# Kernel tuning notes

Measured on AMD Instinct MI355X. Metric: run time of the kernel, lower is better.

Reference implementation:

```python
import jax, jax.numpy as jnp
import numpy as np

COMMITMENT_LOSS_WEIGHT = 0.25


def setup_inputs() -> dict:
    key = jax.random.key(0)
    k1, k2 = jax.random.split(key)
    B, H, W, C = 64, 32, 32, 256
    D, K = H * W, 1024  # embedding_dim = H*W per the rearrange+reshape in call()
    x = jax.random.normal(k1, (B, H, W, C), dtype=jnp.float32)
    # Orthogonal initializer (like tf.keras.initializers.Orthogonal) via QR
    E = jnp.linalg.qr(jax.random.normal(k2, (D, K), dtype=jnp.float32))[0]
    return {"x": x, "embeddings": E.astype(jnp.float32)}


def reference(x, embeddings):
    B, H, W, C = x.shape
    D = H * W  # embedding_dim
    # einops: 'b h w c -> b c (h w)'
    cont = jnp.transpose(x, (0, 3, 1, 2)).reshape(B, C, D)
    flat = cont.reshape(-1, D)  # [B*C, D]
    # squared L2 distances via norm + matmul (as in get_discretised)
    dists = (jnp.sum(flat * flat, axis=1, keepdims=True)
             + jnp.sum(embeddings * embeddings, axis=0)
             - 2.0 * (flat @ embeddings))  # [B*C, K]
    idx = jnp.argmin(dists, axis=1)  # [B*C]
    # one_hot @ embeddings.T == direct gather of codebook columns
    quantised = embeddings.T[idx].reshape(B, C, D)
    codebook_loss = jnp.mean((jax.lax.stop_gradient(cont) - quantised) ** 2)
    commitment_loss = COMMITMENT_LOSS_WEIGHT * jnp.mean(
        (cont - jax.lax.stop_gradient(quantised)) ** 2)
    loss = codebook_loss + commitment_loss  # layer add_loss terms, summed
    # einops: 'b c (h w) -> b h w c'
    q_bhwc = jnp.transpose(quantised.reshape(B, C, H, W), (0, 2, 3, 1))
    discretised = idx.reshape(-1, C)  # [B, C]
    # straight-through estimator
    q_out = x + jax.lax.stop_gradient(q_bhwc - x)
    return q_out, discretised, loss
```

## Files before the change

### kernel.cpp

```cpp
#include <hip/hip_runtime.h>
#include <float.h>
#include <stdint.h>

#define B_   64
#define C_   256
#define D_   1024
#define K_   1024
#define M_   16384
#define NX_  16777216
#define DISC_OFF NX_
#define LOSS_OFF (NX_ + M_)

typedef _Float16 h8 __attribute__((ext_vector_type(8)));
typedef float    f4 __attribute__((ext_vector_type(4)));

#define XSCALE 512.0f
#define ESCALE 2048.0f
#define DOT_UNSCALE_2 (2.0f / 1048576.0f)

#define WS_EH  0
#define WS_EL  524288
#define WS_CN  1048576
#define WS_PCN 1049600
#define WS_PV  1180672
#define WS_PI  1246208

__device__ __forceinline__ void async16(const _Float16* g, _Float16* l) {
    __builtin_amdgcn_global_load_lds(
        (const __attribute__((address_space(1))) unsigned int*)g,
        (__attribute__((address_space(3))) unsigned int*)l, 16, 0, 0);
}

__global__ __launch_bounds__(256) void split_kernel(const float* __restrict__ x,
                                                    const float* __restrict__ E,
                                                    _Float16* __restrict__ Xh,
                                                    _Float16* __restrict__ Xl,
                                                    _Float16* __restrict__ Eh,
                                                    _Float16* __restrict__ El,
                                                    float* __restrict__ pcn) {
    const int bid = blockIdx.x;
    if (bid < 512) {
        const int tid = bid * 256 + threadIdx.x;
        const int n   = tid & 1023;
        const int o   = tid >> 10;
        const int d0  = o * 8;
        h8 hh, ll;
        float s = 0.f;
        #pragma unroll
        for (int i = 0; i < 8; ++i) {
            const float v = E[(size_t)(d0 + i) * K_ + n];
            s = fmaf(v, v, s);
            const float vs = v * ESCALE;
            const _Float16 h = (_Float16)vs;
            hh[i] = h;
            ll[i] = (_Float16)(vs - (float)h);
        }
        pcn[o * K_ + n] = s;
        const int nt   = n >> 4;
        const int kt   = o >> 2;
        const int lane = (n & 15) + (o & 3) * 16;
        const size_t off = ((size_t)(nt * 32 + kt) * 64 + lane) * 8;
        *(h8*)(Eh + off) = hh;
        *(h8*)(El + off) = ll;
    } else {
        const int tid = (bid - 512) * 256 + threadIdx.x;
        const int m   = tid & 16383;
        const int o   = tid >> 14;
        const int b   = m >> 8, c = m & 255;
        const int d0  = o * 8;
        const float* xp = x + ((size_t)(b * 1024 + d0) * 256) + c;
        h8 hh, ll;
        #pragma unroll
        for (int i = 0; i < 8; ++i) {
            const float v  = xp[(size_t)i * 256];
            const float vs = v * XSCALE;
            const _Float16 h = (_Float16)vs;
            hh[i] = h;
            ll[i] = (_Float16)(vs - (float)h);
        }
        const int mt   = m >> 4;
        const int kt   = o >> 2;
        const int lane = (m & 15) + (o & 3) * 16;
        const size_t off = ((size_t)(mt * 32 + kt) * 64 + lane) * 8;
        *(h8*)(Xh + off) = hh;
        *(h8*)(Xl + off) = ll;
    }
}

__global__ __launch_bounds__(256) void colnorm2_kernel(const float* __restrict__ pcn,
                                                       float* __restrict__ cn,
                                                       float* __restrict__ loss_slot) {
    const int k = blockIdx.x * 256 + threadIdx.x;
    float s = 0.f;
    for (int i = 0; i < 128; ++i) s += pcn[i * K_ + k];
    cn[k] = s;
    if (k == 0) *loss_slot = 0.0f;
}

__global__ __launch_bounds__(512, 2) void gemm_argmin_kernel(
        const _Float16* __restrict__ Xh, const _Float16* __restrict__ Xl,
        const _Float16* __restrict__ Eh, const _Float16* __restrict__ El,
        const float* __restrict__ cn,
        float* __restrict__ pV, int* __restrict__ pI) {
    extern __shared__ _Float16 smem[];
    _Float16* Ab0 = smem;
    _Float16* Ab1 = smem + 8192;
    _Float16* Bb0 = smem + 16384;
    _Float16* Bb1 = smem + 32768;
    float* cV = (float*)(smem + 49152);
    int*   cI = (int*)(cV + 512);

    const int t    = threadIdx.x;
    const int rt   = blockIdx.x >> 2;
    const int ct   = blockIdx.x & 3;
    const int wave = t >> 6, lane = t & 63;
    const int lo16 = lane & 15, hi4 = lane >> 4;
    const int mq   = (wave & 1) * 64;
    const int nq   = (wave >> 1) * 64;
    const int mt0  = rt * 8, nt0 = ct * 16;
    const int n0g  = ct * 256;

    const _Float16* src[6];
    _Float16* dst0[6];
    _Float16* dst1[6];
    #pragma unroll
    for (int i = 0; i < 6; ++i) {
        const int id = wave * 6 + i;
        if (id < 16) {
            const int plane = id >> 3, mt = id & 7;
            src[i]  = (plane ? Xl : Xh) + ((size_t)(mt0 + mt) * 32) * 512 + lane * 8;
            dst0[i] = Ab0 + (plane * 8 + mt) * 512 + lane * 8;
            dst1[i] = Ab1 + (plane * 8 + mt) * 512 + lane * 8;
        } else {
            const int q = id - 16;
            const int plane = q >> 4, nt = q & 15;
            src[i]  = (plane ? El : Eh) + ((size_t)(nt0 + nt) * 32) * 512 + lane * 8;
            dst0[i] = Bb0 + (plane * 16 + nt) * 512 + lane * 8;
            dst1[i] = Bb1 + (plane * 16 + nt) * 512 + lane * 8;
        }
    }

    f4 acc[4][4];
    const f4 zero = {0.f, 0.f, 0.f, 0.f};
    #pragma unroll
    for (int i = 0; i < 4; ++i)
        #pragma unroll
        for (int j = 0; j < 4; ++j) acc[i][j] = zero;

    #pragma unroll
    for (int i = 0; i < 6; ++i) async16(src[i], dst0[i]);

    for (int s = 0; s < 32; ++s) {
        const int cur = s & 1;
        __syncthreads();
        if (s + 1 < 32) {
            #pragma unroll
            for (int i = 0; i < 6; ++i)
                async16(src[i] + (size_t)(s + 1) * 512, cur ? dst0[i] : dst1[i]);
        }
        const _Float16* Abuf = cur ? Ab1 : Ab0;
        const _Float16* Bbuf = cur ? Bb1 : Bb0;

        h8 Bf[2][4];
        #pragma unroll
        for (int tn = 0; tn < 4; ++tn) {
            const int tixn = (nq >> 4) + tn;
            Bf[0][tn] = *(const h8*)&Bbuf[tixn * 512 + lane * 8];
            Bf[1][tn] = *(const h8*)&Bbuf[(16 + tixn) * 512 + lane * 8];
        }
        #pragma unroll
        for (int tm = 0; tm < 4; ++tm) {
            const int tixm = (mq >> 4) + tm;
            const h8 Ah = *(const h8*)&Abuf[tixm * 512 + lane * 8];
            const h8 Al = *(const h8*)&Abuf[(8 + tixm) * 512 + lane * 8];
            #pragma unroll
            for (int tn = 0; tn < 4; ++tn) {
                acc[tm][tn] = __builtin_amdgcn_mfma_f32_16x16x32_f16(Ah, Bf[0][tn], acc[tm][tn], 0, 0, 0);
                acc[tm][tn] = __builtin_amdgcn_mfma_f32_16x16x32_f16(Ah, Bf[1][tn], acc[tm][tn], 0, 0, 0);
                acc[tm][tn] = __builtin_amdgcn_mfma_f32_16x16x32_f16(Al, Bf[0][tn], acc[tm][tn], 0, 0, 0);
            }
        }
    }

    float cnv[4];
    #pragma unroll
    for (int tn = 0; tn < 4; ++tn) cnv[tn] = cn[n0g + nq + tn * 16 + lo16];

    #pragma unroll
    for (int tm = 0; tm < 4; ++tm) {
        #pragma unroll
        for (int r = 0; r < 4; ++r) {
            float bv = FLT_MAX;
            int   bi = 0;
            #pragma unroll
            for (int tn = 0; tn < 4; ++tn) {
                const float v = cnv[tn] - acc[tm][tn][r] * DOT_UNSCALE_2;
                if (v < bv) { bv = v; bi = nq + tn * 16 + lo16; }
            }
            #pragma unroll
            for (int msk = 1; msk < 16; msk <<= 1) {
                const float ov = __shfl_xor(bv, msk, 64);
                const int   oi = __shfl_xor(bi, msk, 64);
                if (ov < bv || (ov == bv && oi < bi)) { bv = ov; bi = oi; }
            }
            if (lo16 == 0) {
                const int row = mq + tm * 16 + hi4 * 4 + r;
                const int g   = wave >> 1;
                cV[row * 4 + g] = bv;
                cI[row * 4 + g] = bi;
            }
        }
    }
    __syncthreads();
    if (t < 128) {
        float bv = FLT_MAX;
        int   bi = 0;
        #pragma unroll
        for (int g = 0; g < 4; ++g) {
            const float v = cV[t * 4 + g];
            const int   i = cI[t * 4 + g];
            if (v < bv || (v == bv && i < bi)) { bv = v; bi = i; }
        }
        const int row = rt * 128 + t;
        pV[row * 4 + ct] = bv;
        pI[row * 4 + ct] = n0g + bi;
    }
}

__global__ __launch_bounds__(256) void reduce_kernel(const float* __restrict__ pV,
                                                     const int* __restrict__ pI,
                                                     float* __restrict__ disc) {
    const int rid = blockIdx.x * 256 + threadIdx.x;
    float bv = FLT_MAX;
    int   bi = 0;
    #pragma unroll
    for (int c = 0; c < 4; ++c) {
        const float v = pV[rid * 4 + c];
        const int   i = pI[rid * 4 + c];
        if (v < bv || (v == bv && i < bi)) { bv = v; bi = i; }
    }
    disc[rid] = (float)bi;
}

__global__ __launch_bounds__(256) void finalize_kernel(const float* __restrict__ x,
                                                       const float* __restrict__ E,
                                                       const float* __restrict__ discf,
                                                       float* __restrict__ out,
                                                       float* __restrict__ loss) {
    __shared__ float Erow[1024];
    const int t = threadIdx.x;
    const int d = blockIdx.x;
    *(float4*)&Erow[t * 4] = *(const float4*)(E + (size_t)d * K_ + t * 4);
    __syncthreads();

    const int bl = t >> 6;
    const int c4 = (t & 63) * 4;
    float lsum = 0.f;
    #pragma unroll 4
    for (int bg = 0; bg < 64; bg += 4) {
        const int b = bg + bl;
        const float4 id4 = *(const float4*)(discf + b * 256 + c4);
        const size_t xoff = ((size_t)(b * 1024 + d) << 8) + c4;
        const float4 xv = *(const float4*)(x + xoff);
        const float e0 = Erow[(int)id4.x];
        const float e1 = Erow[(int)id4.y];
        const float e2 = Erow[(int)id4.z];
        const float e3 = Erow[(int)id4.w];
        float4 qv;
        qv.x = xv.x + (e0 - xv.x);
        qv.y = xv.y + (e1 - xv.y);
        qv.z = xv.z + (e2 - xv.z);
        qv.w = xv.w + (e3 - xv.w);
        *(float4*)(out + xoff) = qv;
        const float d0 = xv.x - e0, d1 = xv.y - e1, d2 = xv.z - e2, d3 = xv.w - e3;
        lsum += fmaf(d0, d0, fmaf(d1, d1, fmaf(d2, d2, d3 * d3)));
    }

    #pragma unroll
    for (int off = 32; off > 0; off >>= 1)
        lsum += __shfl_down(lsum, off);
    __shared__ float wsum[4];
    if ((t & 63) == 0) wsum[t >> 6] = lsum;
    __syncthreads();
    if (t == 0) {
        const float s = (wsum[0] + wsum[1]) + (wsum[2] + wsum[3]);
        atomicAdd(loss, s * (1.25f / 16777216.0f));
    }
}

extern "C" void kernel_launch(void* const* d_in, const int* in_sizes, int n_in,
                              void* d_out, int out_size, void* d_ws, size_t ws_size,
                              hipStream_t stream) {
    (void)in_sizes; (void)n_in; (void)out_size; (void)ws_size;
    const float* x = (const float*)d_in[0];
    const float* E = (const float*)d_in[1];
    float* out = (float*)d_out;
    float* ws  = (float*)d_ws;

    _Float16* Eh = (_Float16*)(ws + WS_EH);
    _Float16* El = (_Float16*)(ws + WS_EL);
    float* cn    = ws + WS_CN;
    float* pcn   = ws + WS_PCN;
    float* pV    = ws + WS_PV;
    int*   pI    = (int*)(ws + WS_PI);

    _Float16* Xh = (_Float16*)out;
    _Float16* Xl = (_Float16*)out + NX_;
    float* disc  = out + DISC_OFF;
    float* loss  = out + LOSS_OFF;

    static bool attr_set = false;
    hipFuncSetAttribute((const void*)gemm_argmin_kernel,
                        hipFuncAttributeMaxDynamicSharedMemorySize, 102400);
    (void)attr_set;

    split_kernel   <<<8704, 256, 0, stream>>>(x, E, Xh, Xl, Eh, El, pcn);
    colnorm2_kernel<<<4,    256, 0, stream>>>(pcn, cn, loss);
    gemm_argmin_kernel<<<512, 512, 102400, stream>>>(Xh, Xl, Eh, El, cn, pV, pI);
    reduce_kernel  <<<64,   256, 0, stream>>>(pV, pI, disc);
    finalize_kernel<<<1024, 256, 0, stream>>>(x, E, disc, out, loss);
}
```

Measured before the change: 249.2 us.

## Load codebook fragments directly to registers, stage only X tiles in LDS

The GEMM-argmin kernel no longer stages the E (codebook) tiles through shared memory. Each wave loads its own B fragments straight from global memory into registers, double-buffered, while only the A tiles go through LDS via async copies. The K loop is unrolled by two with explicit ping-pong buffers. This cuts LDS use from 100 KB of dynamic memory to about 36 KB of static memory, which may allow more blocks per CU and removes the LDS round trip for B. The cost is that B is fetched redundantly by the waves that share the same N columns, and it adds register pressure under launch_bounds(512,2).

Result: slower. 265.9 us (+6.7%).

```diff
diff --git a/kernel.cpp b/kernel.cpp
--- a/kernel.cpp
+++ b/kernel.cpp
@@ -102,13 +102,9 @@
         const _Float16* __restrict__ Eh, const _Float16* __restrict__ El,
         const float* __restrict__ cn,
         float* __restrict__ pV, int* __restrict__ pI) {
-    extern __shared__ _Float16 smem[];
-    _Float16* Ab0 = smem;
-    _Float16* Ab1 = smem + 8192;
-    _Float16* Bb0 = smem + 16384;
-    _Float16* Bb1 = smem + 32768;
-    float* cV = (float*)(smem + 49152);
-    int*   cI = (int*)(cV + 512);
+    __shared__ _Float16 Ab[2][16 * 512];
+    __shared__ float cV[128 * 4];
+    __shared__ int   cI[128 * 4];
 
     const int t    = threadIdx.x;
     const int rt   = blockIdx.x >> 2;
@@ -119,25 +115,26 @@
     const int nq   = (wave >> 1) * 64;
     const int mt0  = rt * 8, nt0 = ct * 16;
     const int n0g  = ct * 256;
-
-    const _Float16* src[6];
-    _Float16* dst0[6];
-    _Float16* dst1[6];
-    #pragma unroll
-    for (int i = 0; i < 6; ++i) {
-        const int id = wave * 6 + i;
-        if (id < 16) {
-            const int plane = id >> 3, mt = id & 7;
-            src[i]  = (plane ? Xl : Xh) + ((size_t)(mt0 + mt) * 32) * 512 + lane * 8;
-            dst0[i] = Ab0 + (plane * 8 + mt) * 512 + lane * 8;
-            dst1[i] = Ab1 + (plane * 8 + mt) * 512 + lane * 8;
-        } else {
-            const int q = id - 16;
-            const int plane = q >> 4, nt = q & 15;
-            src[i]  = (plane ? El : Eh) + ((size_t)(nt0 + nt) * 32) * 512 + lane * 8;
-            dst0[i] = Bb0 + (plane * 16 + nt) * 512 + lane * 8;
-            dst1[i] = Bb1 + (plane * 16 + nt) * 512 + lane * 8;
-        }
+    const int amq  = mq >> 4;
+    const int lane8 = lane * 8;
+
+    const _Float16* srcA[2];
+    _Float16* dstA[2][2];
+    #pragma unroll
+    for (int i = 0; i < 2; ++i) {
+        const int id = wave * 2 + i;
+        const int plane = id >> 3, mt = id & 7;
+        srcA[i] = (plane ? Xl : Xh) + ((size_t)(mt0 + mt) * 32) * 512 + lane8;
+        dstA[0][i] = &Ab[0][(plane * 8 + mt) * 512 + lane8];
+        dstA[1][i] = &Ab[1][(plane * 8 + mt) * 512 + lane8];
+    }
+
+    const _Float16* srcB[2][4];
+    #pragma unroll
+    for (int tn = 0; tn < 4; ++tn) {
+        const int nt = nt0 + (nq >> 4) + tn;
+        srcB[0][tn] = Eh + ((size_t)nt * 32) * 512 + lane8;
+        srcB[1][tn] = El + ((size_t)nt * 32) * 512 + lane8;
     }
 
     f4 acc[4][4];
@@ -147,40 +144,55 @@
         #pragma unroll
         for (int j = 0; j < 4; ++j) acc[i][j] = zero;
 
-    #pragma unroll
-    for (int i = 0; i < 6; ++i) async16(src[i], dst0[i]);
-
-    for (int s = 0; s < 32; ++s) {
-        const int cur = s & 1;
+    h8 Bf0[2][4], Bf1[2][4];
+
+    #pragma unroll
+    for (int i = 0; i < 2; ++i) async16(srcA[i], dstA[0][i]);
+    #pragma unroll
+    for (int p = 0; p < 2; ++p)
+        #pragma unroll
+        for (int tn = 0; tn < 4; ++tn) Bf0[p][tn] = *(const h8*)(srcB[p][tn]);
+
+    #define COMPUTE(ABUF, BF)                                                            \
+        do {                                                                             \
+            _Pragma("unroll")                                                            \
+            for (int tm = 0; tm < 4; ++tm) {                                             \
+                const h8 Ah = *(const h8*)&(ABUF)[(amq + tm) * 512 + lane8];             \
+                const h8 Al = *(const h8*)&(ABUF)[(8 + amq + tm) * 512 + lane8];         \
+                _Pragma("unroll")                                                        \
+                for (int tn = 0; tn < 4; ++tn) {                                         \
+                    acc[tm][tn] = __builtin_amdgcn_mfma_f32_16x16x32_f16(Ah, (BF)[0][tn], acc[tm][tn], 0, 0, 0); \
+                    acc[tm][tn] = __builtin_amdgcn_mfma_f32_16x16x32_f16(Ah, (BF)[1][tn], acc[tm][tn], 0, 0, 0); \
+                    acc[tm][tn] = __builtin_amdgcn_mfma_f32_16x16x32_f16(Al, (BF)[0][tn], acc[tm][tn], 0, 0, 0); \
+                }                                                                        \
+            }                                                                            \
+        } while (0)
+
+    for (int s = 0; s < 32; s += 2) {
         __syncthreads();
-        if (s + 1 < 32) {
-            #pragma unroll
-            for (int i = 0; i < 6; ++i)
-                async16(src[i] + (size_t)(s + 1) * 512, cur ? dst0[i] : dst1[i]);
-        }
-        const _Float16* Abuf = cur ? Ab1 : Ab0;
-        const _Float16* Bbuf = cur ? Bb1 : Bb0;
-
-        h8 Bf[2][4];
-        #pragma unroll
-        for (int tn = 0; tn < 4; ++tn) {
-            const int tixn = (nq >> 4) + tn;
-            Bf[0][tn] = *(const h8*)&Bbuf[tixn * 512 + lane * 8];
-            Bf[1][tn] = *(const h8*)&Bbuf[(16 + tixn) * 512 + lane * 8];
-        }
-        #pragma unroll
-        for (int tm = 0; tm < 4; ++tm) {
-            const int tixm = (mq >> 4) + tm;
-            const h8 Ah = *(const h8*)&Abuf[tixm * 512 + lane * 8];
-            const h8 Al = *(const h8*)&Abuf[(8 + tixm) * 512 + lane * 8];
-            #pragma unroll
-            for (int tn = 0; tn < 4; ++tn) {
-                acc[tm][tn] = __builtin_amdgcn_mfma_f32_16x16x32_f16(Ah, Bf[0][tn], acc[tm][tn], 0, 0, 0);
-                acc[tm][tn] = __builtin_amdgcn_mfma_f32_16x16x32_f16(Ah, Bf[1][tn], acc[tm][tn], 0, 0, 0);
-                acc[tm][tn] = __builtin_amdgcn_mfma_f32_16x16x32_f16(Al, Bf[0][tn], acc[tm][tn], 0, 0, 0);
-            }
-        }
-    }
+        {
+            #pragma unroll
+            for (int i = 0; i < 2; ++i) async16(srcA[i] + (size_t)(s + 1) * 512, dstA[1][i]);
+            #pragma unroll
+            for (int p = 0; p < 2; ++p)
+                #pragma unroll
+                for (int tn = 0; tn < 4; ++tn)
+                    Bf1[p][tn] = *(const h8*)(srcB[p][tn] + (size_t)(s + 1) * 512);
+        }
+        COMPUTE(Ab[0], Bf0);
+        __syncthreads();
+        if (s + 2 < 32) {
+            #pragma unroll
+            for (int i = 0; i < 2; ++i) async16(srcA[i] + (size_t)(s + 2) * 512, dstA[0][i]);
+            #pragma unroll
+            for (int p = 0; p < 2; ++p)
+                #pragma unroll
+                for (int tn = 0; tn < 4; ++tn)
+                    Bf0[p][tn] = *(const h8*)(srcB[p][tn] + (size_t)(s + 2) * 512);
+        }
+        COMPUTE(Ab[1], Bf1);
+    }
+    #undef COMPUTE
 
     float cnv[4];
     #pragma unroll
@@ -309,14 +321,9 @@
     float* disc  = out + DISC_OFF;
     float* loss  = out + LOSS_OFF;
 
-    static bool attr_set = false;
-    hipFuncSetAttribute((const void*)gemm_argmin_kernel,
-                        hipFuncAttributeMaxDynamicSharedMemorySize, 102400);
-    (void)attr_set;
-
     split_kernel   <<<8704, 256, 0, stream>>>(x, E, Xh, Xl, Eh, El, pcn);
     colnorm2_kernel<<<4,    256, 0, stream>>>(pcn, cn, loss);
-    gemm_argmin_kernel<<<512, 512, 102400, stream>>>(Xh, Xl, Eh, El, cn, pV, pI);
+    gemm_argmin_kernel<<<512, 512, 0, stream>>>(Xh, Xl, Eh, El, cn, pV, pI);
     reduce_kernel  <<<64,   256, 0, stream>>>(pV, pI, disc);
     finalize_kernel<<<1024, 256, 0, stream>>>(x, E, disc, out, loss);
 }
```
